# Optimization experiments

Hardware: AMD Instinct MI355X
Metric: run time of the kernel (lower is better)

## Reference

```python
import jax, jax.numpy as jnp
import numpy as np
import math

HEADS = 8
KSIZE = 25  # decomposition moving-average window

def moving_avg(x, k):
    # x: [B, S, E]; replicate-pad last axis by (k-1)//2 on both sides, window mean (stride 1)
    p = (k - 1) // 2
    xp = jnp.pad(x, ((0, 0), (0, 0), (p, p)), mode='edge')
    cs = jnp.cumsum(xp, axis=-1)
    cs = jnp.concatenate([jnp.zeros_like(cs[..., :1]), cs], axis=-1)
    return (cs[..., k:] - cs[..., :-k]) / k

def decompose(x, k):
    trend = moving_avg(x, k)
    return x - trend, trend

def setup_inputs() -> dict:
    key = jax.random.key(0)
    ks = jax.random.split(key, 16)
    B, S, E = 4, 2048, 256
    H = HEADS
    D = E // H
    FF = 4 * E
    OUT = E
    s = 0.02
    inp = {
        'x': jax.random.normal(ks[0], (B, S, E), dtype=jnp.float32),
        'mask': jnp.ones((B, 1, 1, S), dtype=jnp.int32),
        'wq': jax.random.normal(ks[1], (D, D), dtype=jnp.float32) * s,
        'wk': jax.random.normal(ks[2], (D, D), dtype=jnp.float32) * s,
        'wv': jax.random.normal(ks[3], (D, D), dtype=jnp.float32) * s,
        'w_out': jax.random.normal(ks[4], (E, E), dtype=jnp.float32) * s,
        'b_out': jnp.zeros((E,), dtype=jnp.float32),
        'ff_w1': jax.random.normal(ks[5], (E, FF), dtype=jnp.float32) * s,
        'ff_b1': jnp.zeros((FF,), dtype=jnp.float32),
        'ff_w2': jax.random.normal(ks[6], (FF, E), dtype=jnp.float32) * s,
        'ff_b2': jnp.zeros((E,), dtype=jnp.float32),
        'pr_w1': jax.random.normal(ks[7], (E, FF), dtype=jnp.float32) * s,
        'pr_b1': jnp.zeros((FF,), dtype=jnp.float32),
        'pr_w2': jax.random.normal(ks[8], (FF, OUT), dtype=jnp.float32) * s,
        'pr_b2': jnp.zeros((OUT,), dtype=jnp.float32),
    }
    return inp

def reference(x, mask, wq, wk, wv, w_out, b_out, ff_w1, ff_b1, ff_w2, ff_b2, pr_w1, pr_b1, pr_w2, pr_b2):
    B, S, E = x.shape
    H = HEADS
    D = E // H
    # multihead attention (per-head shared projections, scale by sqrt(embed_size))
    xh = x.reshape(B, S, H, D)
    q = xh @ wq
    k = xh @ wk
    v = xh @ wv
    scores = jnp.einsum('nqhd,nkhd->nhqk', q, k) / jnp.float32(math.sqrt(E))
    scores = jnp.where(mask == 0, jnp.float32(-1e20), scores)
    attn = jax.nn.softmax(scores, axis=-1)
    attn_out = jnp.einsum('nhqk,nkhd->nqhd', attn, v).reshape(B, S, E)
    attn_out = attn_out @ w_out + b_out
    # residual (dropout is identity at inference)
    x = x + attn_out
    # first decomposition: keep seasonal part
    y, _ = decompose(x, KSIZE)
    # FFN
    z = jnp.maximum(y @ ff_w1 + ff_b1, 0.0) @ ff_w2 + ff_b2
    s = y + z
    # second decomposition
    s, _ = decompose(s, KSIZE)
    # projection FFN
    out = jnp.maximum(s @ pr_w1 + pr_b1, 0.0) @ pr_w2 + pr_b2
    return out
```

## Files before the change

kernel.cpp:

```cpp
#include <hip/hip_runtime.h>
#include <hip/hip_bf16.h>
#include <math.h>

#define B_   4
#define S_   2048
#define E_   256
#define H_   8
#define D_   32
#define FF_  1024
#define NTOK (B_*S_)

typedef __attribute__((ext_vector_type(8))) short short8;
typedef __attribute__((ext_vector_type(4))) float f32x4;
typedef __attribute__((ext_vector_type(4))) unsigned u32x4;
typedef __hip_bfloat16 bf16;

#define QSCALE 0.09016844005556021f

__device__ __forceinline__ unsigned short round_bf16(float a) {
    unsigned ua = __builtin_bit_cast(unsigned, a);
    return (unsigned short)((ua + 0x7fffu + ((ua >> 16) & 1u)) >> 16);
}
__device__ __forceinline__ unsigned cvtpk_bf16(float lo, float hi) {
    unsigned r;
    asm("v_cvt_pk_bf16_f32 %0, %1, %2" : "=v"(r) : "v"(lo), "v"(hi));
    return r;
}
__device__ __forceinline__ float fexp2(float x) {
    float r;
    asm("v_exp_f32 %0, %1" : "=v"(r) : "v"(x));
    return r;
}
__device__ __forceinline__ void gld16(const short* g, short* l) {
    __builtin_amdgcn_global_load_lds(
        (const __attribute__((address_space(1))) unsigned int*)g,
        (__attribute__((address_space(3))) unsigned int*)l, 16, 0, 0);
}
__device__ __forceinline__ short8 lds_frag(const short* base, int r, int c16) {
    return *(const short8*)(base + r*64 + (((c16) ^ (r & 7)) << 3));
}

__global__ __launch_bounds__(256) void qkv_prep_kernel(
    const float* __restrict__ x,
    const float* __restrict__ wq, const float* __restrict__ wk, const float* __restrict__ wv,
    bf16* __restrict__ q, bf16* __restrict__ k, unsigned short* __restrict__ vt,
    const float* __restrict__ w_out, const float* __restrict__ ff_w1,
    const float* __restrict__ ff_w2, const float* __restrict__ pr_w1,
    const float* __restrict__ pr_w2,
    unsigned short* __restrict__ woT, unsigned short* __restrict__ f1T,
    unsigned short* __restrict__ f2T, unsigned short* __restrict__ p1T,
    unsigned short* __restrict__ p2T,
    const int* __restrict__ mask, int* __restrict__ mflags)
{
    const int bid = blockIdx.x;
    if (bid >= 512) {
        const int pb = bid - 512;
        if (pb >= 1088) {
            const int t = threadIdx.x;
            if (t < 128) {
                const int* p = mask + (t >> 5)*S_ + (t & 31)*64;
                int any0 = 0;
                #pragma unroll
                for (int i = 0; i < 16; ++i) {
                    const int4 vv = *(const int4*)(p + i*4);
                    if (!(vv.x && vv.y && vv.z && vv.w)) any0 = 1;
                }
                mflags[t] = any0;
            }
            return;
        }
        const float* w; unsigned short* wt; int K, N, idx;
        if (pb < 64)       { w = w_out; wt = woT; K = E_;  N = E_;  idx = pb; }
        else if (pb < 320) { w = ff_w1; wt = f1T; K = E_;  N = FF_; idx = pb - 64; }
        else if (pb < 576) { w = ff_w2; wt = f2T; K = FF_; N = E_;  idx = pb - 320; }
        else if (pb < 832) { w = pr_w1; wt = p1T; K = E_;  N = FF_; idx = pb - 576; }
        else               { w = pr_w2; wt = p2T; K = FF_; N = E_;  idx = pb - 832; }
        const int nb = N/32;
        const int n0 = (idx % nb)*32, k0 = (idx / nb)*32;
        __shared__ float tile[32][33];
        const int c = threadIdx.x & 31, r0 = threadIdx.x >> 5;
        #pragma unroll
        for (int i = 0; i < 4; ++i)
            tile[r0 + 8*i][c] = w[(size_t)(k0 + r0 + 8*i)*N + n0 + c];
        __syncthreads();
        #pragma unroll
        for (int i = 0; i < 4; ++i)
            wt[(size_t)(n0 + r0 + 8*i)*K + k0 + c] = round_bf16(tile[c][r0 + 8*i]);
        return;
    }
    __shared__ float wqs[D_*D_], wks[D_*D_], wvs[D_*D_];
    __shared__ float xs[16][E_];
    __shared__ unsigned short vsh[16*256];
    const int tid = threadIdx.x;
    for (int i = tid; i < D_*D_; i += 256) {
        wqs[i] = wq[i]; wks[i] = wk[i]; wvs[i] = wv[i];
    }
    const int tok0 = bid * 16;
    #pragma unroll
    for (int i = 0; i < 16; ++i)
        xs[i][tid] = x[(size_t)(tok0 + i)*E_ + tid];
    __syncthreads();
    const int h = tid >> 5, d = tid & 31;
    const int b  = tok0 >> 11;
    const int s0 = tok0 & (S_-1);
    for (int t = 0; t < 16; ++t) {
        float aq = 0.f, ak = 0.f, av = 0.f;
        #pragma unroll
        for (int i = 0; i < D_; ++i) {
            const float xv = xs[t][h*D_ + i];
            aq += xv * wqs[i*D_ + d];
            ak += xv * wks[i*D_ + d];
            av += xv * wvs[i*D_ + d];
        }
        const int s = s0 + t;
        const int u = s & 63;
        const int sp = (s & ~63) | (((u>>5)&1)*32 + ((u>>2)&1)*16 + ((u>>3)&3)*4 + (u&3));
        const size_t base = (size_t)(b*H_ + h)*S_;
        q[(base + s )*D_ + d] = __float2bfloat16(aq * QSCALE);
        k[(base + sp)*D_ + d] = __float2bfloat16(ak);
        vsh[t*256 + tid] = round_bf16(av);
    }
    __syncthreads();
    unsigned vv[8];
    #pragma unroll
    for (int i = 0; i < 8; ++i) {
        const unsigned lo = vsh[(2*i    )*256 + tid];
        const unsigned hi = vsh[(2*i + 1)*256 + tid];
        vv[i] = lo | (hi << 16);
    }
    unsigned short* dst = vt + ((size_t)((b*H_ + h)*D_ + d))*S_ + s0;
    *(u32x4*)(dst)     = (u32x4){vv[0], vv[1], vv[2], vv[3]};
    *(u32x4*)(dst + 8) = (u32x4){vv[4], vv[5], vv[6], vv[7]};
}

__global__ __launch_bounds__(256) void attn_mfma_kernel(
    const short* __restrict__ qg, const short* __restrict__ kg,
    const short* __restrict__ vtg, const int* __restrict__ mask,
    const int* __restrict__ mflags, unsigned short* __restrict__ attn_out)
{
    __shared__ alignas(16) short lk[2][64*32];
    __shared__ alignas(16) short lv[2][32*64];

    const int tid  = threadIdx.x;
    const int lane = tid & 63;
    const int wid  = tid >> 6;
    const int c    = lane & 15;
    const int g    = lane >> 4;
    const int p    = ((int)blockIdx.x & 7)*64 + ((int)blockIdx.x >> 3);
    const int bh   = p >> 4;
    const int qt   = p & 15;
    const int b    = bh >> 3;
    const int h    = bh & 7;
    const int q0   = qt*128 + wid*32;

    const short* qrow = qg + ((size_t)bh*S_ + q0 + c)*D_ + g*8;
    const short8 qfA = *(const short8*)(qrow);
    const short8 qfB = *(const short8*)(qrow + 16*D_);
    const short* kbase = kg  + (size_t)bh*S_*D_;
    const short* vbase = vtg + (size_t)bh*D_*S_;
    const int*   mrow  = mask + b*S_;

    const int fl = (lane < 32) ? mflags[b*32 + lane] : 0;
    const unsigned long long mbits = __ballot(fl != 0);

    const short* sbase; int soff0, soff1, sinc, dchunk0;
    if (wid < 2) {
        const int R0 = wid*32 + (lane >> 2);
        const int R1 = R0 + 16;
        const int s  = lane & 3;
        soff0 = R0*D_ + ((s ^ ((R0 >> 1) & 3)) << 3);
        soff1 = R1*D_ + ((s ^ ((R1 >> 1) & 3)) << 3);
        sbase = kbase; sinc = 64*D_;
        dchunk0 = wid*1024;
    } else {
        const int r0 = (wid - 2)*16 + (lane >> 3);
        const int r1 = r0 + 8;
        const int s  = lane & 7;
        soff0 = r0*S_ + ((s ^ (r0 & 7)) << 3);
        soff1 = r1*S_ + ((s ^ (r1 & 7)) << 3);
        sbase = vbase; sinc = 64;
        dchunk0 = (wid - 2)*1024;
    }

    const int kaddr = c*D_ + ((g ^ ((c >> 1) & 3)) << 3);
    const int va0   = c*64 + ((g       ^ (c & 7)) << 3);
    const int va1   = c*64 + (((g + 4) ^ (c & 7)) << 3);
    const f32x4 zero = {0.f,0.f,0.f,0.f};
    const short8 ones = { (short)0x3F80, (short)0x3F80, (short)0x3F80, (short)0x3F80,
                          (short)0x3F80, (short)0x3F80, (short)0x3F80, (short)0x3F80 };
    f32x4 oA0 = zero, oA1 = zero, oB0 = zero, oB1 = zero;
    f32x4 lAacc = zero, lBacc = zero;

    {
        short* d0 = (wid < 2 ? &lk[0][0] : &lv[0][0]) + dchunk0;
        gld16(sbase + soff0, d0);
        gld16(sbase + soff1, d0 + 512);
    }
    __syncthreads();

    int buf = 0;
    for (int t = 0; t < 32; ++t) {
        if (t < 31) {
            const short* sp = sbase + (size_t)(t + 1)*sinc;
            short* d0 = (wid < 2 ? &lk[buf ^ 1][0] : &lv[buf ^ 1][0]) + dchunk0;
            gld16(sp + soff0, d0);
            gld16(sp + soff1, d0 + 512);
        }
        const short* LK = &lk[buf][0];
        const short* LV = &lv[buf][0];
        const short8 kf0 = *(const short8*)(LK + kaddr);
        const short8 kf1 = *(const short8*)(LK + kaddr + 512);
        const short8 kf2 = *(const short8*)(LK + kaddr + 1024);
        const short8 kf3 = *(const short8*)(LK + kaddr + 1536);
        __builtin_amdgcn_s_setprio(1);
        f32x4 sA0 = __builtin_amdgcn_mfma_f32_16x16x32_bf16(kf0, qfA, zero, 0, 0, 0);
        f32x4 sA1 = __builtin_amdgcn_mfma_f32_16x16x32_bf16(kf1, qfA, zero, 0, 0, 0);
        f32x4 sA2 = __builtin_amdgcn_mfma_f32_16x16x32_bf16(kf2, qfA, zero, 0, 0, 0);
        f32x4 sA3 = __builtin_amdgcn_mfma_f32_16x16x32_bf16(kf3, qfA, zero, 0, 0, 0);
        f32x4 sB0 = __builtin_amdgcn_mfma_f32_16x16x32_bf16(kf0, qfB, zero, 0, 0, 0);
        f32x4 sB1 = __builtin_amdgcn_mfma_f32_16x16x32_bf16(kf1, qfB, zero, 0, 0, 0);
        f32x4 sB2 = __builtin_amdgcn_mfma_f32_16x16x32_bf16(kf2, qfB, zero, 0, 0, 0);
        f32x4 sB3 = __builtin_amdgcn_mfma_f32_16x16x32_bf16(kf3, qfB, zero, 0, 0, 0);
        __builtin_amdgcn_s_setprio(0);
        if ((mbits >> t) & 1ull) {
            const int kb = t*64 + 8*g;
            #pragma unroll
            for (int r = 0; r < 4; ++r) {
                if (mrow[kb      + r] == 0) { sA0[r] = -1e20f; sB0[r] = -1e20f; }
                if (mrow[kb + 4  + r] == 0) { sA1[r] = -1e20f; sB1[r] = -1e20f; }
                if (mrow[kb + 32 + r] == 0) { sA2[r] = -1e20f; sB2[r] = -1e20f; }
                if (mrow[kb + 36 + r] == 0) { sA3[r] = -1e20f; sB3[r] = -1e20f; }
            }
        }
        f32x4 pA0, pA1, pA2, pA3, pB0, pB1, pB2, pB3;
        #pragma unroll
        for (int r = 0; r < 4; ++r) {
            pA0[r] = fexp2(sA0[r]); pA1[r] = fexp2(sA1[r]);
            pA2[r] = fexp2(sA2[r]); pA3[r] = fexp2(sA3[r]);
            pB0[r] = fexp2(sB0[r]); pB1[r] = fexp2(sB1[r]);
            pB2[r] = fexp2(sB2[r]); pB3[r] = fexp2(sB3[r]);
        }
        const short8 pafA0 = __builtin_bit_cast(short8,
            (u32x4){ cvtpk_bf16(pA0[0],pA0[1]), cvtpk_bf16(pA0[2],pA0[3]),
                     cvtpk_bf16(pA1[0],pA1[1]), cvtpk_bf16(pA1[2],pA1[3]) });
        const short8 pafA1 = __builtin_bit_cast(short8,
            (u32x4){ cvtpk_bf16(pA2[0],pA2[1]), cvtpk_bf16(pA2[2],pA2[3]),
                     cvtpk_bf16(pA3[0],pA3[1]), cvtpk_bf16(pA3[2],pA3[3]) });
        const short8 pafB0 = __builtin_bit_cast(short8,
            (u32x4){ cvtpk_bf16(pB0[0],pB0[1]), cvtpk_bf16(pB0[2],pB0[3]),
                     cvtpk_bf16(pB1[0],pB1[1]), cvtpk_bf16(pB1[2],pB1[3]) });
        const short8 pafB1 = __builtin_bit_cast(short8,
            (u32x4){ cvtpk_bf16(pB2[0],pB2[1]), cvtpk_bf16(pB2[2],pB2[3]),
                     cvtpk_bf16(pB3[0],pB3[1]), cvtpk_bf16(pB3[2],pB3[3]) });
        const short8 vf0 = *(const short8*)(LV + va0);
        const short8 vf1 = *(const short8*)(LV + va1);
        const short8 vf2 = *(const short8*)(LV + va0 + 1024);
        const short8 vf3 = *(const short8*)(LV + va1 + 1024);
        __builtin_amdgcn_s_setprio(1);
        oA0 = __builtin_amdgcn_mfma_f32_16x16x32_bf16(vf0, pafA0, oA0, 0, 0, 0);
        oA0 = __builtin_amdgcn_mfma_f32_16x16x32_bf16(vf1, pafA1, oA0, 0, 0, 0);
        oA1 = __builtin_amdgcn_mfma_f32_16x16x32_bf16(vf2, pafA0, oA1, 0, 0, 0);
        oA1 = __builtin_amdgcn_mfma_f32_16x16x32_bf16(vf3, pafA1, oA1, 0, 0, 0);
        oB0 = __builtin_amdgcn_mfma_f32_16x16x32_bf16(vf0, pafB0, oB0, 0, 0, 0);
        oB0 = __builtin_amdgcn_mfma_f32_16x16x32_bf16(vf1, pafB1, oB0, 0, 0, 0);
        oB1 = __builtin_amdgcn_mfma_f32_16x16x32_bf16(vf2, pafB0, oB1, 0, 0, 0);
        oB1 = __builtin_amdgcn_mfma_f32_16x16x32_bf16(vf3, pafB1, oB1, 0, 0, 0);
        lAacc = __builtin_amdgcn_mfma_f32_16x16x32_bf16(ones, pafA0, lAacc, 0, 0, 0);
        lAacc = __builtin_amdgcn_mfma_f32_16x16x32_bf16(ones, pafA1, lAacc, 0, 0, 0);
        lBacc = __builtin_amdgcn_mfma_f32_16x16x32_bf16(ones, pafB0, lBacc, 0, 0, 0);
        lBacc = __builtin_amdgcn_mfma_f32_16x16x32_bf16(ones, pafB1, lBacc, 0, 0, 0);
        __builtin_amdgcn_s_setprio(0);
        __syncthreads();
        buf ^= 1;
    }
    const float invA = 1.0f / lAacc[0], invB = 1.0f / lBacc[0];
    unsigned short* orowA = attn_out + ((size_t)b*S_ + q0 + c)*E_ + h*D_ + g*4;
    unsigned short* orowB = orowA + (size_t)16*E_;
    uint2 a0, a1, b0, b1;
    a0.x = cvtpk_bf16(oA0[0]*invA, oA0[1]*invA); a0.y = cvtpk_bf16(oA0[2]*invA, oA0[3]*invA);
    a1.x = cvtpk_bf16(oA1[0]*invA, oA1[1]*invA); a1.y = cvtpk_bf16(oA1[2]*invA, oA1[3]*invA);
    b0.x = cvtpk_bf16(oB0[0]*invB, oB0[1]*invB); b0.y = cvtpk_bf16(oB0[2]*invB, oB0[3]*invB);
    b1.x = cvtpk_bf16(oB1[0]*invB, oB1[1]*invB); b1.y = cvtpk_bf16(oB1[2]*invB, oB1[3]*invB);
    *(uint2*)(orowA)      = a0;
    *(uint2*)(orowA + 16) = a1;
    *(uint2*)(orowB)      = b0;
    *(uint2*)(orowB + 16) = b1;
}

template<int WF32, int WBF16>
__global__ __launch_bounds__(256) void mgemm_dec_kernel(
    const short* __restrict__ A, const short* __restrict__ WT,
    const float* __restrict__ bias, const float* __restrict__ R,
    float* __restrict__ o32, unsigned short* __restrict__ ob,
    int M, int K)
{
    __shared__ alignas(16) short stage[2][18432];
    float* dec = (float*)&stage[0][0];
    const int t = threadIdx.x, w = t >> 6, lane = t & 63;
    const int col = lane & 15, grp = lane >> 4;
    const int wm = w >> 1, wn = w & 1;
    const int nwg = gridDim.x;
    const int bm = ((int)blockIdx.x & 7)*(nwg >> 3) + ((int)blockIdx.x >> 3);
    const int arow = t >> 3, ac = t & 7;

    f32x4 acc[8];
    #pragma unroll
    for (int j = 0; j < 8; ++j) acc[j] = (f32x4){0.f,0.f,0.f,0.f};

    {
        const int row = arow;
        gld16(A + (size_t)(bm*32 + row)*K + ((ac ^ (row & 7)) << 3),
              &stage[0][0] + w*512);
        #pragma unroll
        for (int b2 = 0; b2 < 8; ++b2) {
            const int rowb = b2*32 + arow;
            gld16(WT + (size_t)rowb*K + ((ac ^ (rowb & 7)) << 3),
                  &stage[0][2048] + b2*2048 + w*512);
        }
    }
    __syncthreads();

    int buf = 0;
    for (int kb = 0; kb < K; kb += 64) {
        if (kb + 64 < K) {
            const int row = arow;
            gld16(A + (size_t)(bm*32 + row)*K + kb + 64 + ((ac ^ (row & 7)) << 3),
                  &stage[buf ^ 1][0] + w*512);
            #pragma unroll
            for (int b2 = 0; b2 < 8; ++b2) {
                const int rowb = b2*32 + arow;
                gld16(WT + (size_t)rowb*K + kb + 64 + ((ac ^ (rowb & 7)) << 3),
                      &stage[buf ^ 1][2048] + b2*2048 + w*512);
            }
        }
        const short* As_ = &stage[buf][0];
        const short* Bs_ = &stage[buf][2048];
        #pragma unroll
        for (int s = 0; s < 2; ++s) {
            const short8 af = lds_frag(As_, wm*16 + col, s*4 + grp);
            #pragma unroll
            for (int fc = 0; fc < 8; ++fc) {
                const short8 bf_ = lds_frag(Bs_, wn*128 + fc*16 + col, s*4 + grp);
                acc[fc] = __builtin_amdgcn_mfma_f32_16x16x32_bf16(af, bf_, acc[fc], 0, 0, 0);
            }
        }
        __syncthreads();
        buf ^= 1;
    }

    #pragma unroll
    for (int fc = 0; fc < 8; ++fc) {
        const int n = wn*128 + fc*16 + col;
        const float bs = bias[n];
        #pragma unroll
        for (int reg = 0; reg < 4; ++reg) {
            const int m = wm*16 + grp*4 + reg;
            float v = acc[fc][reg] + bs;
            v += R[(size_t)(bm*32 + m)*E_ + n];
            dec[m*261 + n] = v;
        }
    }
    __syncthreads();
    const int row = t & 31, ch = t >> 5;
    const int c0 = ch * 32;
    const float* dr = dec + row*261;
    float sum = 0.f;
    #pragma unroll
    for (int j = -12; j <= 12; ++j) {
        int jj = c0 + j;
        jj = jj < 0 ? 0 : (jj > 255 ? 255 : jj);
        sum += dr[jj];
    }
    float res[32];
    #pragma unroll
    for (int i = 0; i < 32; ++i) {
        const int cc = c0 + i;
        res[i] = dr[cc] - sum * (1.0f/25.0f);
        const int hi = cc + 13 > 255 ? 255 : cc + 13;
        const int lo = cc - 12 < 0 ? 0 : cc - 12;
        sum += dr[hi] - dr[lo];
    }
    const size_t gro = (size_t)(bm*32 + row)*E_ + c0;
    if (WF32) {
        #pragma unroll
        for (int i = 0; i < 8; ++i)
            *(f32x4*)(o32 + gro + i*4) = (f32x4){res[4*i], res[4*i+1], res[4*i+2], res[4*i+3]};
    }
    if (WBF16) {
        #pragma unroll
        for (int i = 0; i < 4; ++i) {
            u32x4 pk;
            #pragma unroll
            for (int j = 0; j < 4; ++j)
                pk[j] = cvtpk_bf16(res[8*i + 2*j], res[8*i + 2*j + 1]);
            *(u32x4*)(ob + gro + i*8) = pk;
        }
    }
}

template<int BM, int BN, int DB, int RELU, int RESID, int WF32, int WBF16>
__global__ __launch_bounds__(256) void mgemm_kernel(
    const short* __restrict__ A, const short* __restrict__ WT,
    const float* __restrict__ bias, const float* __restrict__ R,
    float* __restrict__ C32, unsigned short* __restrict__ Cb,
    int M, int N, int K)
{
    constexpr int FR = BM / 32;
    constexpr int FC = BN / 32;
    constexpr int NB = DB ? 2 : 1;
    __shared__ alignas(16) short As[NB][BM*64];
    __shared__ alignas(16) short Bs[NB][BN*64];
    const int t = threadIdx.x, w = t >> 6, lane = t & 63;
    const int col = lane & 15, grp = lane >> 4;
    const int wm = w >> 1, wn = w & 1;
    const int gx = N / BN;
    const int nwg = gridDim.x;
    const int lin = ((int)blockIdx.x & 7)*(nwg >> 3) + ((int)blockIdx.x >> 3);
    const int bm = lin / gx, bn = lin % gx;
    const int arow = t >> 3, ac = t & 7;

    f32x4 acc[FR][FC];
    #pragma unroll
    for (int i = 0; i < FR; ++i)
        #pragma unroll
        for (int j = 0; j < FC; ++j) acc[i][j] = (f32x4){0.f,0.f,0.f,0.f};

    if (DB) {
        #pragma unroll
        for (int b2 = 0; b2 < BM/32; ++b2) {
            const int row = b2*32 + arow;
            gld16(A + (size_t)(bm*BM + row)*K + ((ac ^ (row & 7)) << 3),
                  &As[0][0] + b2*2048 + w*512);
        }
        #pragma unroll
        for (int b2 = 0; b2 < BN/32; ++b2) {
            const int row = b2*32 + arow;
            gld16(WT + (size_t)(bn*BN + row)*K + ((ac ^ (row & 7)) << 3),
                  &Bs[0][0] + b2*2048 + w*512);
        }
        __syncthreads();
        int buf = 0;
        for (int kb = 0; kb < K; kb += 64) {
            if (kb + 64 < K) {
                #pragma unroll
                for (int b2 = 0; b2 < BM/32; ++b2) {
                    const int row = b2*32 + arow;
                    gld16(A + (size_t)(bm*BM + row)*K + kb + 64 + ((ac ^ (row & 7)) << 3),
                          &As[buf ^ 1][0] + b2*2048 + w*512);
                }
                #pragma unroll
                for (int b2 = 0; b2 < BN/32; ++b2) {
                    const int row = b2*32 + arow;
                    gld16(WT + (size_t)(bn*BN + row)*K + kb + 64 + ((ac ^ (row & 7)) << 3),
                          &Bs[buf ^ 1][0] + b2*2048 + w*512);
                }
            }
            #pragma unroll
            for (int s = 0; s < 2; ++s) {
                short8 af[FR], bf_[FC];
                #pragma unroll
                for (int fr = 0; fr < FR; ++fr)
                    af[fr] = lds_frag(&As[buf][0], wm*(BM/2) + fr*16 + col, s*4 + grp);
                #pragma unroll
                for (int fc = 0; fc < FC; ++fc)
                    bf_[fc] = lds_frag(&Bs[buf][0], wn*(BN/2) + fc*16 + col, s*4 + grp);
                #pragma unroll
                for (int fr = 0; fr < FR; ++fr)
                    #pragma unroll
                    for (int fc = 0; fc < FC; ++fc)
                        acc[fr][fc] = __builtin_amdgcn_mfma_f32_16x16x32_bf16(af[fr], bf_[fc], acc[fr][fc], 0, 0, 0);
            }
            __syncthreads();
            buf ^= 1;
        }
    } else {
        for (int kb = 0; kb < K; kb += 64) {
            #pragma unroll
            for (int b2 = 0; b2 < BM/32; ++b2) {
                const int row = b2*32 + arow;
                gld16(A + (size_t)(bm*BM + row)*K + kb + ((ac ^ (row & 7)) << 3),
                      &As[0][0] + b2*2048 + w*512);
            }
            #pragma unroll
            for (int b2 = 0; b2 < BN/32; ++b2) {
                const int row = b2*32 + arow;
                gld16(WT + (size_t)(bn*BN + row)*K + kb + ((ac ^ (row & 7)) << 3),
                      &Bs[0][0] + b2*2048 + w*512);
            }
            __syncthreads();
            #pragma unroll
            for (int s = 0; s < 2; ++s) {
                short8 af[FR], bf_[FC];
                #pragma unroll
                for (int fr = 0; fr < FR; ++fr)
                    af[fr] = lds_frag(&As[0][0], wm*(BM/2) + fr*16 + col, s*4 + grp);
                #pragma unroll
                for (int fc = 0; fc < FC; ++fc)
                    bf_[fc] = lds_frag(&Bs[0][0], wn*(BN/2) + fc*16 + col, s*4 + grp);
                #pragma unroll
                for (int fr = 0; fr < FR; ++fr)
                    #pragma unroll
                    for (int fc = 0; fc < FC; ++fc)
                        acc[fr][fc] = __builtin_amdgcn_mfma_f32_16x16x32_bf16(af[fr], bf_[fc], acc[fr][fc], 0, 0, 0);
            }
            __syncthreads();
        }
    }

    #pragma unroll
    for (int fc = 0; fc < FC; ++fc) {
        const int n = bn*BN + wn*(BN/2) + fc*16 + col;
        const float bs = bias[n];
        #pragma unroll
        for (int fr = 0; fr < FR; ++fr) {
            #pragma unroll
            for (int reg = 0; reg < 4; ++reg) {
                const int m = bm*BM + wm*(BM/2) + fr*16 + grp*4 + reg;
                float v = acc[fr][fc][reg] + bs;
                if (RELU) v = fmaxf(v, 0.f);
                if (RESID) v += R[(size_t)m*N + n];
                if (WF32) C32[(size_t)m*N + n] = v;
                if (WBF16) Cb[(size_t)m*N + n] = round_bf16(v);
            }
        }
    }
}

extern "C" void kernel_launch(void* const* d_in, const int* in_sizes, int n_in,
                              void* d_out, int out_size, void* d_ws, size_t ws_size,
                              hipStream_t stream) {
    const float* x     = (const float*)d_in[0];
    const int*   mask  = (const int*)  d_in[1];
    const float* wq    = (const float*)d_in[2];
    const float* wk    = (const float*)d_in[3];
    const float* wv    = (const float*)d_in[4];
    const float* w_out = (const float*)d_in[5];
    const float* b_out = (const float*)d_in[6];
    const float* ff_w1 = (const float*)d_in[7];
    const float* ff_b1 = (const float*)d_in[8];
    const float* ff_w2 = (const float*)d_in[9];
    const float* ff_b2 = (const float*)d_in[10];
    const float* pr_w1 = (const float*)d_in[11];
    const float* pr_b1 = (const float*)d_in[12];
    const float* pr_w2 = (const float*)d_in[13];
    const float* pr_b2 = (const float*)d_in[14];
    float* out = (float*)d_out;

    char* ws = (char*)d_ws;
    const size_t MB = 1024ull*1024ull;
    const size_t KB = 1024ull;
    bf16*  qb    = (bf16*)(ws + 0*MB);
    bf16*  kbf   = (bf16*)(ws + 4*MB);
    bf16*  vtb   = (bf16*)(ws + 12*MB);
    unsigned short* attnb = (unsigned short*)(ws + 16*MB);
    float* y32   = (float*)(ws + 28*MB);
    unsigned short* yb  = (unsigned short*)(ws + 36*MB);
    unsigned short* h1  = (unsigned short*)(ws + 0*MB);
    unsigned short* s2b = (unsigned short*)(ws + 16*MB);
    unsigned short* h2  = (unsigned short*)(ws + 0*MB);
    unsigned short* woT = (unsigned short*)(ws + 40*MB);
    unsigned short* f1T = (unsigned short*)(ws + 40*MB + 128*KB);
    unsigned short* f2T = (unsigned short*)(ws + 40*MB + 640*KB);
    unsigned short* p1T = (unsigned short*)(ws + 40*MB + 1152*KB);
    unsigned short* p2T = (unsigned short*)(ws + 40*MB + 1664*KB);
    int*            mfl = (int*)           (ws + 40*MB + 2176*KB);

    qkv_prep_kernel<<<1601, 256, 0, stream>>>(x, wq, wk, wv, qb, kbf,
                                              (unsigned short*)vtb,
                                              w_out, ff_w1, ff_w2, pr_w1, pr_w2,
                                              woT, f1T, f2T, p1T, p2T, mask, mfl);
    attn_mfma_kernel<<<B_*H_*S_/128, 256, 0, stream>>>(
        (const short*)qb, (const short*)kbf, (const short*)vtb, mask, mfl, attnb);
    mgemm_dec_kernel<1,1><<<NTOK/32, 256, 0, stream>>>(
        (const short*)attnb, (const short*)woT, b_out, x, y32, yb, NTOK, E_);
    mgemm_kernel<128,128,0,1,0,0,1><<<(NTOK/128)*(FF_/128), 256, 0, stream>>>(
        (const short*)yb, (const short*)f1T, ff_b1, nullptr, nullptr, h1, NTOK, FF_, E_);
    mgemm_dec_kernel<0,1><<<NTOK/32, 256, 0, stream>>>(
        (const short*)h1, (const short*)f2T, ff_b2, y32, nullptr, s2b, NTOK, FF_);
    mgemm_kernel<128,128,0,1,0,0,1><<<(NTOK/128)*(FF_/128), 256, 0, stream>>>(
        (const short*)s2b, (const short*)p1T, pr_b1, nullptr, nullptr, h2, NTOK, FF_, E_);
    mgemm_kernel<64,64,1,0,0,1,0><<<(NTOK/64)*(E_/64), 256, 0, stream>>>(
        (const short*)h2, (const short*)p2T, pr_b2, nullptr, out, nullptr, NTOK, E_, FF_);
}
```

Baseline: 120.0 us.

## Split attention key range across two wave groups with LDS reduction

Doubles the attention block to 512 threads and assigns each half of the waves to one half of the key sequence, halving the serial key-tile loop per block. Each half loads its own K/V tiles into separate LDS buffers, and at the end the second half writes its partial output and row-sum accumulators to LDS for the first half to combine before normalizing. This shortens the per-block critical path, but adds LDS traffic, an extra barrier and the register and occupancy costs of larger blocks.

```diff
diff --git a/kernel.cpp b/kernel.cpp
--- a/kernel.cpp
+++ b/kernel.cpp
@@ -133,25 +133,27 @@
     *(u32x4*)(dst + 8) = (u32x4){vv[4], vv[5], vv[6], vv[7]};
 }
 
-__global__ __launch_bounds__(256) void attn_mfma_kernel(
+__global__ __launch_bounds__(512) void attn_mfma_kernel(
     const short* __restrict__ qg, const short* __restrict__ kg,
     const short* __restrict__ vtg, const int* __restrict__ mask,
     const int* __restrict__ mflags, unsigned short* __restrict__ attn_out)
 {
-    __shared__ alignas(16) short lk[2][64*32];
-    __shared__ alignas(16) short lv[2][32*64];
+    __shared__ alignas(16) short lk[2][2][2048];
+    __shared__ alignas(16) short lv[2][2][2048];
 
     const int tid  = threadIdx.x;
     const int lane = tid & 63;
     const int wid  = tid >> 6;
     const int c    = lane & 15;
     const int g    = lane >> 4;
+    const int half = wid >> 2;
+    const int qs   = wid & 3;
     const int p    = ((int)blockIdx.x & 7)*64 + ((int)blockIdx.x >> 3);
     const int bh   = p >> 4;
     const int qt   = p & 15;
     const int b    = bh >> 3;
     const int h    = bh & 7;
-    const int q0   = qt*128 + wid*32;
+    const int q0   = qt*128 + qs*32;
 
     const short* qrow = qg + ((size_t)bh*S_ + q0 + c)*D_ + g*8;
     const short8 qfA = *(const short8*)(qrow);
@@ -163,23 +165,27 @@
     const int fl = (lane < 32) ? mflags[b*32 + lane] : 0;
     const unsigned long long mbits = __ballot(fl != 0);
 
-    const short* sbase; int soff0, soff1, sinc, dchunk0;
-    if (wid < 2) {
-        const int R0 = wid*32 + (lane >> 2);
+    const int sthalf = (wid >> 1) & 1;
+    const int subw   = wid & 1;
+    const short* sbase; int soff0, soff1, sinc, dchunk;
+    if (wid < 4) {
+        const int R0 = subw*32 + (lane >> 2);
         const int R1 = R0 + 16;
         const int s  = lane & 3;
         soff0 = R0*D_ + ((s ^ ((R0 >> 1) & 3)) << 3);
         soff1 = R1*D_ + ((s ^ ((R1 >> 1) & 3)) << 3);
-        sbase = kbase; sinc = 64*D_;
-        dchunk0 = wid*1024;
+        sbase = kbase + (size_t)sthalf*16*64*D_;
+        sinc  = 64*D_;
+        dchunk = subw*1024;
     } else {
-        const int r0 = (wid - 2)*16 + (lane >> 3);
+        const int r0 = subw*16 + (lane >> 3);
         const int r1 = r0 + 8;
         const int s  = lane & 7;
         soff0 = r0*S_ + ((s ^ (r0 & 7)) << 3);
         soff1 = r1*S_ + ((s ^ (r1 & 7)) << 3);
-        sbase = vbase; sinc = 64;
-        dchunk0 = (wid - 2)*1024;
+        sbase = vbase + sthalf*16*64;
+        sinc  = 64;
+        dchunk = subw*1024;
     }
 
     const int kaddr = c*D_ + ((g ^ ((c >> 1) & 3)) << 3);
@@ -192,22 +198,22 @@
     f32x4 lAacc = zero, lBacc = zero;
 
     {
-        short* d0 = (wid < 2 ? &lk[0][0] : &lv[0][0]) + dchunk0;
+        short* d0 = (wid < 4 ? &lk[0][sthalf][0] : &lv[0][sthalf][0]) + dchunk;
         gld16(sbase + soff0, d0);
         gld16(sbase + soff1, d0 + 512);
     }
     __syncthreads();
 
     int buf = 0;
-    for (int t = 0; t < 32; ++t) {
-        if (t < 31) {
+    for (int t = 0; t < 16; ++t) {
+        if (t < 15) {
             const short* sp = sbase + (size_t)(t + 1)*sinc;
-            short* d0 = (wid < 2 ? &lk[buf ^ 1][0] : &lv[buf ^ 1][0]) + dchunk0;
+            short* d0 = (wid < 4 ? &lk[buf ^ 1][sthalf][0] : &lv[buf ^ 1][sthalf][0]) + dchunk;
             gld16(sp + soff0, d0);
             gld16(sp + soff1, d0 + 512);
         }
-        const short* LK = &lk[buf][0];
-        const short* LV = &lv[buf][0];
+        const short* LK = &lk[buf][half][0];
+        const short* LV = &lv[buf][half][0];
         const short8 kf0 = *(const short8*)(LK + kaddr);
         const short8 kf1 = *(const short8*)(LK + kaddr + 512);
         const short8 kf2 = *(const short8*)(LK + kaddr + 1024);
@@ -222,8 +228,9 @@
         f32x4 sB2 = __builtin_amdgcn_mfma_f32_16x16x32_bf16(kf2, qfB, zero, 0, 0, 0);
         f32x4 sB3 = __builtin_amdgcn_mfma_f32_16x16x32_bf16(kf3, qfB, zero, 0, 0, 0);
         __builtin_amdgcn_s_setprio(0);
-        if ((mbits >> t) & 1ull) {
-            const int kb = t*64 + 8*g;
+        const int tt = half*16 + t;
+        if ((mbits >> tt) & 1ull) {
+            const int kb = tt*64 + 8*g;
             #pragma unroll
             for (int r = 0; r < 4; ++r) {
                 if (mrow[kb      + r] == 0) { sA0[r] = -1e20f; sB0[r] = -1e20f; }
@@ -273,18 +280,42 @@
         __syncthreads();
         buf ^= 1;
     }
-    const float invA = 1.0f / lAacc[0], invB = 1.0f / lBacc[0];
-    unsigned short* orowA = attn_out + ((size_t)b*S_ + q0 + c)*E_ + h*D_ + g*4;
-    unsigned short* orowB = orowA + (size_t)16*E_;
-    uint2 a0, a1, b0, b1;
-    a0.x = cvtpk_bf16(oA0[0]*invA, oA0[1]*invA); a0.y = cvtpk_bf16(oA0[2]*invA, oA0[3]*invA);
-    a1.x = cvtpk_bf16(oA1[0]*invA, oA1[1]*invA); a1.y = cvtpk_bf16(oA1[2]*invA, oA1[3]*invA);
-    b0.x = cvtpk_bf16(oB0[0]*invB, oB0[1]*invB); b0.y = cvtpk_bf16(oB0[2]*invB, oB0[3]*invB);
-    b1.x = cvtpk_bf16(oB1[0]*invB, oB1[1]*invB); b1.y = cvtpk_bf16(oB1[2]*invB, oB1[3]*invB);
-    *(uint2*)(orowA)      = a0;
-    *(uint2*)(orowA + 16) = a1;
-    *(uint2*)(orowB)      = b0;
-    *(uint2*)(orowB + 16) = b1;
+    float* oM = (float*)&lk[0][0][0];
+    float* lM = (float*)&lv[0][0][0];
+    if (half == 1) {
+        float* o = oM + (qs*64 + lane)*16;
+        #pragma unroll
+        for (int r = 0; r < 4; ++r) {
+            o[r]      = oA0[r];
+            o[4 + r]  = oA1[r];
+            o[8 + r]  = oB0[r];
+            o[12 + r] = oB1[r];
+        }
+        lM[(qs*64 + lane)*2 + 0] = lAacc[0];
+        lM[(qs*64 + lane)*2 + 1] = lBacc[0];
+    }
+    __syncthreads();
+    if (half == 0) {
+        const float* o = oM + (qs*64 + lane)*16;
+        const float lA = lAacc[0] + lM[(qs*64 + lane)*2 + 0];
+        const float lB = lBacc[0] + lM[(qs*64 + lane)*2 + 1];
+        const float invA = 1.0f / lA, invB = 1.0f / lB;
+        unsigned short* orowA = attn_out + ((size_t)b*S_ + q0 + c)*E_ + h*D_ + g*4;
+        unsigned short* orowB = orowA + (size_t)16*E_;
+        uint2 a0, a1, b0, b1;
+        a0.x = cvtpk_bf16((oA0[0]+o[0])*invA,  (oA0[1]+o[1])*invA);
+        a0.y = cvtpk_bf16((oA0[2]+o[2])*invA,  (oA0[3]+o[3])*invA);
+        a1.x = cvtpk_bf16((oA1[0]+o[4])*invA,  (oA1[1]+o[5])*invA);
+        a1.y = cvtpk_bf16((oA1[2]+o[6])*invA,  (oA1[3]+o[7])*invA);
+        b0.x = cvtpk_bf16((oB0[0]+o[8])*invB,  (oB0[1]+o[9])*invB);
+        b0.y = cvtpk_bf16((oB0[2]+o[10])*invB, (oB0[3]+o[11])*invB);
+        b1.x = cvtpk_bf16((oB1[0]+o[12])*invB, (oB1[1]+o[13])*invB);
+        b1.y = cvtpk_bf16((oB1[2]+o[14])*invB, (oB1[3]+o[15])*invB);
+        *(uint2*)(orowA)      = a0;
+        *(uint2*)(orowA + 16) = a1;
+        *(uint2*)(orowB)      = b0;
+        *(uint2*)(orowB + 16) = b1;
+    }
 }
 
 template<int WF32, int WBF16>
@@ -569,7 +600,7 @@
                                               (unsigned short*)vtb,
                                               w_out, ff_w1, ff_w2, pr_w1, pr_w2,
                                               woT, f1T, f2T, p1T, p2T, mask, mfl);
-    attn_mfma_kernel<<<B_*H_*S_/128, 256, 0, stream>>>(
+    attn_mfma_kernel<<<B_*H_*S_/128, 512, 0, stream>>>(
         (const short*)qb, (const short*)kbf, (const short*)vtb, mask, mfl, attnb);
     mgemm_dec_kernel<1,1><<<NTOK/32, 256, 0, stream>>>(
         (const short*)attnb, (const short*)woT, b_out, x, y32, yb, NTOK, E_);
```

Result: faster. 112.6 us (-6.2%).
